# Optimization experiments

Hardware: AMD Instinct MI355X
Metric: run time of the kernel (lower is better)

## Reference

```python
import jax, jax.numpy as jnp
import numpy as np

B, T, D = 256, 300, 512


def setup_inputs() -> dict:
    key = jax.random.key(0)
    k1, k2, k3, k4 = jax.random.split(key, 4)
    x = jax.random.normal(k1, (B, T, D), dtype=jnp.float32)
    weights = jax.random.uniform(k2, (B, T, 1), dtype=jnp.float32)
    # learned params: D (log-variance vector, init zero-ish) and chol (upper-triangular, init ~identity)
    D_w = 0.01 * jax.random.normal(k3, (D,), dtype=jnp.float32)
    chol_w = jnp.eye(D, dtype=jnp.float32) + 0.01 * jnp.triu(
        jax.random.normal(k4, (D, D), dtype=jnp.float32), k=1)
    return {"x": x, "weights": weights, "D_w": D_w, "chol_w": chol_w}


def reference(x, weights, D_w, chol_w):
    # weighted first-order stats
    gamma = jnp.sum(x * weights, axis=1)                     # [B, D]
    N = jnp.sum(weights, axis=1, keepdims=True)              # [B, 1, 1]

    var_i = jnp.exp(D_w)                                     # [D]
    cov_i = (chol_w.T * var_i) @ chol_w                      # chol^T diag(var) chol, SPD [D, D]
    prec_i = jnp.linalg.inv(cov_i)[None]                     # [1, D, D]

    eye = jnp.eye(D, dtype=x.dtype)[None]                    # [1, D, D]
    prec = eye + N * prec_i                                  # [B, D, D]

    cov = jnp.linalg.inv(prec)                               # batched inverse [B, D, D]
    cov = 0.5 * (cov + jnp.transpose(cov, (0, 2, 1)))        # symmetrize

    # K.batch_dot(gamma, cov) with default axes contracts gamma dim1 with cov dim2
    mu = jnp.einsum('bd,bed->be', gamma, cov)                # [B, D]

    # upper Cholesky factor: cov = U^T U with U = L^T
    L = jnp.linalg.cholesky(cov)                             # lower [B, D, D]
    chol = jnp.transpose(L, (0, 2, 1))                       # upper [B, D, D]
    sigma = jnp.diagonal(chol, axis1=1, axis2=2)             # [B, D]
    chol = chol / sigma[:, :, None]                          # unit-diagonal rows
    logvar = 2.0 * jnp.log(sigma)                            # [B, D]
    return mu, logvar, chol
```

## Files before the change

### kernel.cpp

```cpp
#include <hip/hip_runtime.h>
#include <math.h>

#define Bn 256
#define Tn 300
#define Nn 512
#define NB 64
#define LDV 68
#define LDA 65

#define TOFF(i,j) ((size_t)((i)*NB)*Nn + (size_t)(j)*NB)

__device__ __forceinline__ void load_tile_f4(const float* __restrict__ g, int tid, float4 r[2]) {
#pragma unroll
  for (int t = 0; t < 2; t++) {
    int q = tid + 512 * t;
    int row = q >> 4, c4 = q & 15;
    r[t] = ((const float4*)(g + (size_t)row * Nn))[c4];
  }
}
__device__ __forceinline__ void store_stage(float* __restrict__ s, int tid, const float4 r[2]) {
#pragma unroll
  for (int t = 0; t < 2; t++) {
    int q = tid + 512 * t;
    int row = q >> 4, c4 = q & 15;
    *((float4*)(s + row * LDV + c4 * 4)) = r[t];
  }
}
__device__ __forceinline__ void mm_nt_sub(const float* __restrict__ sa, const float* __restrict__ sb,
                                          int tr, int tc, float acc[2][4]) {
#pragma unroll 2
  for (int k = 0; k < NB; k += 4) {
    float4 av[2], bv[4];
#pragma unroll
    for (int i = 0; i < 2; i++) av[i] = *(const float4*)(sa + (tr * 2 + i) * LDV + k);
#pragma unroll
    for (int j = 0; j < 4; j++) bv[j] = *(const float4*)(sb + (tc + 16 * j) * LDV + k);
#pragma unroll
    for (int i = 0; i < 2; i++)
#pragma unroll
      for (int j = 0; j < 4; j++)
        acc[i][j] -= av[i].x * bv[j].x + av[i].y * bv[j].y + av[i].z * bv[j].z + av[i].w * bv[j].w;
  }
}

__global__ __launch_bounds__(256) void k_gamma(const float* __restrict__ x,
                                               const float* __restrict__ w,
                                               float* __restrict__ gamma,
                                               float* __restrict__ Nsum) {
  int b = blockIdx.x, tid = threadIdx.x;
  const float2* xb = (const float2*)(x + (size_t)b * Tn * Nn);
  const float* wb = w + b * Tn;
  float gx = 0.f, gy = 0.f, ns = 0.f;
#pragma unroll 4
  for (int t = 0; t < Tn; t++) {
    float wt = wb[t];
    ns += wt;
    float2 v = xb[(size_t)t * 256 + tid];
    gx += v.x * wt;
    gy += v.y * wt;
  }
  float2 g2; g2.x = gx; g2.y = gy;
  ((float2*)(gamma + b * Nn))[tid] = g2;
  if (tid == 0) Nsum[b] = ns;
}

__global__ __launch_bounds__(256) void k_prepC(const float* __restrict__ Dw,
                                               const float* __restrict__ cholw,
                                               float* __restrict__ C) {
  int r = blockIdx.x, tid = threadIdx.x;
  float s = expf(0.5f * Dw[r]);
  for (int c = tid; c < Nn; c += 256)
    C[r * Nn + c] = (c >= r) ? s * cholw[r * Nn + c] : 0.f;
}

__global__ __launch_bounds__(256) void k_cct(const float* __restrict__ C,
                                             float* __restrict__ CCT) {
  __shared__ float Ci[32][33];
  __shared__ float Cj[32][33];
  int tid = threadIdx.x;
  int idx = blockIdx.x, ti = 0, tj;
  if (idx < 136) {
    while (idx >= 16 - ti) { idx -= 16 - ti; ti++; }
    tj = ti + idx;
  } else {
    ti = 2 * (idx - 136) + 1;
    tj = ti - 1;
  }
  int i0 = ti * 32, j0 = tj * 32;
  int m0 = (i0 > j0) ? i0 : j0;
  float acc[4] = {0.f, 0.f, 0.f, 0.f};
  int r = tid >> 3, c0 = tid & 7;
  for (int kt = m0; kt < Nn; kt += 32) {
    __syncthreads();
    for (int q = tid; q < 1024; q += 256) {
      int rr = q >> 5, cc = q & 31;
      Ci[rr][cc] = C[(size_t)(i0 + rr) * Nn + kt + cc];
      Cj[rr][cc] = C[(size_t)(j0 + rr) * Nn + kt + cc];
    }
    __syncthreads();
    for (int k = 0; k < 32; k++) {
      float a = Ci[r][k];
#pragma unroll
      for (int j = 0; j < 4; j++) acc[j] += a * Cj[c0 + 8 * j][k];
    }
  }
#pragma unroll
  for (int j = 0; j < 4; j++)
    CCT[(size_t)(i0 + r) * Nn + j0 + c0 + 8 * j] = acc[j];
}

__global__ __attribute__((amdgpu_waves_per_eu(2)))
__launch_bounds__(512) void k_factor(const float* __restrict__ CCT,
                                     const float* __restrict__ Nsum,
                                     float* __restrict__ AG) {
  const int b = blockIdx.x, tid = threadIdx.x;
  float* A = AG + (size_t)b * Nn * Nn;
  const float Nb = Nsum[b];
  __shared__ __align__(16) float sA[2][NB * LDV];
  __shared__ __align__(16) float sB[2][NB * LDV];
  __shared__ __align__(16) float sVd[NB * LDV];
  __shared__ float sAd[NB * LDA];
  __shared__ float sdg[NB];
  const int tr = tid >> 4, tc = tid & 15;
  float4 ra[2], rb[2];

  for (int j = 7; j >= 0; j--) {
    const int nst = 7 - j;
    float acc[2][4];
    {
      const float* T = CCT + TOFF(j, j);
#pragma unroll
      for (int i = 0; i < 2; i++) {
        const int r = tr * 2 + i;
#pragma unroll
        for (int jj = 0; jj < 4; jj++) {
          const int c = tc + 16 * jj;
          float v = T[(size_t)r * Nn + c];
          if (r == c) v += Nb;
          acc[i][jj] = v;
        }
      }
    }
    if (nst) {
      load_tile_f4(A + TOFF(j, j + 1), tid, ra);
      store_stage(sA[0], tid, ra);
    }
    __syncthreads();
    for (int kk = 0; kk < nst; kk++) {
      const int s = kk & 1;
      if (kk + 1 < nst) load_tile_f4(A + TOFF(j, j + 2 + kk), tid, ra);
      mm_nt_sub(sA[s], sA[s], tr, tc, acc);
      if (kk + 1 < nst) store_stage(sA[s ^ 1], tid, ra);
      __syncthreads();
    }
#pragma unroll
    for (int i = 0; i < 2; i++)
#pragma unroll
      for (int jj = 0; jj < 4; jj++)
        sAd[(tr * 2 + i) * LDA + tc + 16 * jj] = acc[i][jj];
    __syncthreads();
    {
      const int jj = tid & 63, i0 = tid >> 6;
      for (int c = NB - 1; c > 0; --c) {
        float invd = 1.0f / sAd[c * LDA + c];
        if (jj < c) {
          float t = sAd[jj * LDA + c] * invd;
          for (int i = i0; i <= jj; i += 8)
            sAd[i * LDA + jj] -= sAd[i * LDA + c] * t;
        }
        __syncthreads();
      }
      if (tid < NB) sdg[tid] = rsqrtf(sAd[tid * LDA + tid]);
      __syncthreads();
      for (int q = tid; q < NB * NB; q += 512) {
        int r = q >> 6, cc = q & 63;
        if (r <= cc) sAd[r * LDA + cc] *= sdg[cc];
      }
      __syncthreads();
    }
    for (int q = tid; q < NB * LDV; q += 512) sVd[q] = 0.f;
    __syncthreads();
    if (tid < NB) {
      const int c = tid;
      for (int r = c; r >= 0; r--) {
        float s2 = (r == c) ? 1.f : 0.f;
        for (int k = r + 1; k <= c; k++) s2 -= sAd[r * LDA + k] * sVd[k * LDV + c];
        sVd[r * LDV + c] = s2 / sAd[r * LDA + r];
      }
    }
    __syncthreads();
    {
      const int vr = (j < 7) ? 7 : 6, vc = (j < 7) ? j : 0;
      float* Vt = A + TOFF(vr, vc);
      for (int q = tid; q < NB * NB; q += 512) {
        int r = q >> 6, c = q & 63;
        Vt[(size_t)r * Nn + c] = sVd[r * LDV + c];
      }
    }
    for (int i = j - 1; i >= 0; i--) {
      float acc2[2][4];
      {
        const float* T = CCT + TOFF(i, j);
#pragma unroll
        for (int ii = 0; ii < 2; ii++)
#pragma unroll
          for (int jj = 0; jj < 4; jj++)
            acc2[ii][jj] = T[(size_t)(tr * 2 + ii) * Nn + tc + 16 * jj];
      }
      if (nst) {
        load_tile_f4(A + TOFF(i, j + 1), tid, ra);
        load_tile_f4(A + TOFF(j, j + 1), tid, rb);
        store_stage(sA[0], tid, ra);
        store_stage(sB[0], tid, rb);
      }
      __syncthreads();
      for (int kk = 0; kk < nst; kk++) {
        const int s = kk & 1;
        if (kk + 1 < nst) {
          load_tile_f4(A + TOFF(i, j + 2 + kk), tid, ra);
          load_tile_f4(A + TOFF(j, j + 2 + kk), tid, rb);
        }
        mm_nt_sub(sA[s], sB[s], tr, tc, acc2);
        if (kk + 1 < nst) { store_stage(sA[s ^ 1], tid, ra); store_stage(sB[s ^ 1], tid, rb); }
        __syncthreads();
      }
#pragma unroll
      for (int ii = 0; ii < 2; ii++)
#pragma unroll
        for (int jj = 0; jj < 4; jj++)
          sA[0][(tr * 2 + ii) * LDV + tc + 16 * jj] = acc2[ii][jj];
      __syncthreads();
      {
        float out[2][4] = {};
#pragma unroll 2
        for (int k = 0; k < NB; k += 4) {
          float4 av[2], bv[4];
#pragma unroll
          for (int ii = 0; ii < 2; ii++) av[ii] = *(const float4*)(sA[0] + (tr * 2 + ii) * LDV + k);
#pragma unroll
          for (int jj = 0; jj < 4; jj++) bv[jj] = *(const float4*)(sVd + (tc + 16 * jj) * LDV + k);
#pragma unroll
          for (int ii = 0; ii < 2; ii++)
#pragma unroll
            for (int jj = 0; jj < 4; jj++)
              out[ii][jj] += av[ii].x * bv[jj].x + av[ii].y * bv[jj].y +
                             av[ii].z * bv[jj].z + av[ii].w * bv[jj].w;
        }
        float* X = A + TOFF(i, j);
#pragma unroll
        for (int ii = 0; ii < 2; ii++)
#pragma unroll
          for (int jj = 0; jj < 4; jj++)
            X[(size_t)(tr * 2 + ii) * Nn + tc + 16 * jj] = out[ii][jj];
      }
      __syncthreads();
    }
  }
}

__global__ __attribute__((amdgpu_waves_per_eu(2)))
__launch_bounds__(512) void k_solve(const float* __restrict__ C,
                                    float* __restrict__ AG) {
  const int b = blockIdx.x, tid = threadIdx.x;
  float* A = AG + (size_t)b * Nn * Nn;
  __shared__ __align__(16) float sA[2][NB * LDV];
  __shared__ __align__(16) float sB[2][NB * LDV];
  __shared__ __align__(16) float sVd[NB * LDV];
  const int tr = tid >> 4, tc = tid & 15;
  float4 ra[2], rb[2];
  for (int R = 7; R >= 0; R--) {
    {
      const int vr = (R < 7) ? 7 : 6, vc = (R < 7) ? R : 0;
      const float* Vt = A + TOFF(vr, vc);
      __syncthreads();
      for (int q = tid; q < NB * NB; q += 512) {
        int r = q >> 6, c = q & 63;
        sVd[r * LDV + c] = Vt[(size_t)r * Nn + c];
      }
      __syncthreads();
    }
    for (int J = 7; J >= R; J--) {
      const int nst = J - R;
      float acc[2][4];
      {
        const float* T = C + TOFF(R, J);
#pragma unroll
        for (int ii = 0; ii < 2; ii++)
#pragma unroll
          for (int jj = 0; jj < 4; jj++)
            acc[ii][jj] = T[(size_t)(tr * 2 + ii) * Nn + tc + 16 * jj];
      }
      if (nst) {
        load_tile_f4(A + TOFF(R, R + 1), tid, ra);
        load_tile_f4(A + TOFF(R + 1, J), tid, rb);
      }
      __syncthreads();
      if (nst) { store_stage(sA[0], tid, ra); store_stage(sB[0], tid, rb); }
      __syncthreads();
      for (int kk = 0; kk < nst; kk++) {
        const int s = kk & 1;
        if (kk + 1 < nst) {
          load_tile_f4(A + TOFF(R, R + 2 + kk), tid, ra);
          load_tile_f4(A + TOFF(R + 2 + kk, J), tid, rb);
        }
#pragma unroll 2
        for (int k = 0; k < NB; k += 4) {
          float a4[2][4];
#pragma unroll
          for (int ii = 0; ii < 2; ii++) {
            float4 t = *(const float4*)(sA[s] + (tr * 2 + ii) * LDV + k);
            a4[ii][0] = t.x; a4[ii][1] = t.y; a4[ii][2] = t.z; a4[ii][3] = t.w;
          }
#pragma unroll
          for (int k2 = 0; k2 < 4; k2++) {
            float bb[4];
#pragma unroll
            for (int jj = 0; jj < 4; jj++) bb[jj] = sB[s][(k + k2) * LDV + tc + 16 * jj];
#pragma unroll
            for (int ii = 0; ii < 2; ii++)
#pragma unroll
              for (int jj = 0; jj < 4; jj++) acc[ii][jj] -= a4[ii][k2] * bb[jj];
          }
        }
        if (kk + 1 < nst) { store_stage(sA[s ^ 1], tid, ra); store_stage(sB[s ^ 1], tid, rb); }
        __syncthreads();
      }
#pragma unroll
      for (int ii = 0; ii < 2; ii++)
#pragma unroll
        for (int jj = 0; jj < 4; jj++)
          sA[0][(tr * 2 + ii) * LDV + tc + 16 * jj] = acc[ii][jj];
      __syncthreads();
      {
        float out[2][4] = {};
#pragma unroll 2
        for (int k = 0; k < NB; k += 4) {
          float v4[2][4];
#pragma unroll
          for (int ii = 0; ii < 2; ii++) {
            float4 t = *(const float4*)(sVd + (tr * 2 + ii) * LDV + k);
            v4[ii][0] = t.x; v4[ii][1] = t.y; v4[ii][2] = t.z; v4[ii][3] = t.w;
          }
#pragma unroll
          for (int k2 = 0; k2 < 4; k2++) {
            float bb[4];
#pragma unroll
            for (int jj = 0; jj < 4; jj++) bb[jj] = sA[0][(k + k2) * LDV + tc + 16 * jj];
#pragma unroll
            for (int ii = 0; ii < 2; ii++)
#pragma unroll
              for (int jj = 0; jj < 4; jj++) out[ii][jj] += v4[ii][k2] * bb[jj];
          }
        }
        float* G = A + TOFF(R, J);
#pragma unroll
        for (int ii = 0; ii < 2; ii++)
#pragma unroll
          for (int jj = 0; jj < 4; jj++)
            G[(size_t)(tr * 2 + ii) * Nn + tc + 16 * jj] = out[ii][jj];
      }
      __syncthreads();
    }
  }
}

__global__ __launch_bounds__(512) void k_finish(const float* __restrict__ gam,
                                                float* __restrict__ mu,
                                                float* __restrict__ logvar,
                                                float* __restrict__ cholG) {
  int b = blockIdx.x, tid = threadIdx.x;
  float* A = cholG + (size_t)b * Nn * Nn;
  __shared__ float gsh[Nn];
  __shared__ float mup[8][Nn];
  for (int c = tid; c < Nn; c += 512) gsh[c] = gam[b * Nn + c];
  __syncthreads();
  int w = tid >> 6, l = tid & 63;
  float mua[8] = {0.f, 0.f, 0.f, 0.f, 0.f, 0.f, 0.f, 0.f};
  for (int i = w; i < Nn; i += 8) {
    const size_t rowo = (size_t)i * Nn;
    float v[8];
    float s = 0.f;
#pragma unroll
    for (int j = 0; j < 8; j++) {
      int c = (j << 6) + l;
      v[j] = A[rowo + c];
      if (c >= i) s += v[j] * gsh[c];
    }
#pragma unroll
    for (int off = 32; off > 0; off >>= 1) s += __shfl_xor(s, off, 64);
    float d = A[rowo + i];
    float rinv = 1.f / d;
    if (l == 0) logvar[b * Nn + i] = 2.f * logf(d);
#pragma unroll
    for (int j = 0; j < 8; j++) {
      int c = (j << 6) + l;
      if (c >= i) mua[j] += v[j] * s;
      float o = (c > i) ? v[j] * rinv : (c == i ? 1.f : 0.f);
      A[rowo + c] = o;
    }
  }
#pragma unroll
  for (int j = 0; j < 8; j++) mup[w][(j << 6) + l] = mua[j];
  __syncthreads();
  for (int c = tid; c < Nn; c += 512)
    mu[b * Nn + c] = mup[0][c] + mup[1][c] + mup[2][c] + mup[3][c] +
                     mup[4][c] + mup[5][c] + mup[6][c] + mup[7][c];
}

extern "C" void kernel_launch(void* const* d_in, const int* in_sizes, int n_in,
                              void* d_out, int out_size, void* d_ws, size_t ws_size,
                              hipStream_t stream) {
  const float* x = (const float*)d_in[0];
  const float* w = (const float*)d_in[1];
  const float* Dw = (const float*)d_in[2];
  const float* cholw = (const float*)d_in[3];
  float* out = (float*)d_out;
  float* mu = out;
  float* logvar = out + Bn * Nn;
  float* chol = out + 2 * Bn * Nn;
  float* gamma = mu;
  float* Nsum = logvar;
  float* Cm = (float*)d_ws;
  float* CCT = Cm + Nn * Nn;
  (void)in_sizes; (void)n_in; (void)out_size; (void)ws_size;

  k_gamma<<<Bn, 256, 0, stream>>>(x, w, gamma, Nsum);
  k_prepC<<<Nn, 256, 0, stream>>>(Dw, cholw, Cm);
  k_cct<<<144, 256, 0, stream>>>(Cm, CCT);
  k_factor<<<Bn, 512, 0, stream>>>(CCT, Nsum, chol);
  k_solve<<<Bn, 512, 0, stream>>>(Cm, chol);
  k_finish<<<Bn, 512, 0, stream>>>(gamma, mu, logvar, chol);
}
```

Before: 2.255 ms.

## Process two off-diagonal tiles per pass in blocked factor and solve kernels

The blocked inverse-factor and triangular-solve kernels now handle two 64x64 output tiles per loop iteration. Each shared staged tile (the diagonal-row panel in k_factor, the A panel in k_solve) is reused across both accumulations, which cuts barrier count and shared loads per tile. The cost is higher register pressure from double accumulators and more shared memory, since a third staging double-buffer is added and sAd is aliased onto sA1. The trailing __syncthreads after each output write was removed, which relies on the next iteration's barriers to order shared-memory reuse.

```diff
diff --git a/kernel.cpp b/kernel.cpp
--- a/kernel.cpp
+++ b/kernel.cpp
@@ -40,6 +40,115 @@
 #pragma unroll
       for (int j = 0; j < 4; j++)
         acc[i][j] -= av[i].x * bv[j].x + av[i].y * bv[j].y + av[i].z * bv[j].z + av[i].w * bv[j].w;
+  }
+}
+__device__ __forceinline__ void mm_nt_sub2(const float* __restrict__ sa1, const float* __restrict__ sa2,
+                                           const float* __restrict__ sb,
+                                           int tr, int tc, float accA[2][4], float accB[2][4]) {
+#pragma unroll 2
+  for (int k = 0; k < NB; k += 4) {
+    float4 a1[2], a2[2], bv[4];
+#pragma unroll
+    for (int i = 0; i < 2; i++) {
+      a1[i] = *(const float4*)(sa1 + (tr * 2 + i) * LDV + k);
+      a2[i] = *(const float4*)(sa2 + (tr * 2 + i) * LDV + k);
+    }
+#pragma unroll
+    for (int j = 0; j < 4; j++) bv[j] = *(const float4*)(sb + (tc + 16 * j) * LDV + k);
+#pragma unroll
+    for (int i = 0; i < 2; i++)
+#pragma unroll
+      for (int j = 0; j < 4; j++) {
+        accA[i][j] -= a1[i].x * bv[j].x + a1[i].y * bv[j].y + a1[i].z * bv[j].z + a1[i].w * bv[j].w;
+        accB[i][j] -= a2[i].x * bv[j].x + a2[i].y * bv[j].y + a2[i].z * bv[j].z + a2[i].w * bv[j].w;
+      }
+  }
+}
+__device__ __forceinline__ void mm_nt_pos2(const float* __restrict__ t1, const float* __restrict__ t2,
+                                           const float* __restrict__ vd, bool u2,
+                                           int tr, int tc, float o1[2][4], float o2[2][4]) {
+#pragma unroll 2
+  for (int k = 0; k < NB; k += 4) {
+    float4 a1[2], a2[2], bv[4];
+#pragma unroll
+    for (int i = 0; i < 2; i++) {
+      a1[i] = *(const float4*)(t1 + (tr * 2 + i) * LDV + k);
+      if (u2) a2[i] = *(const float4*)(t2 + (tr * 2 + i) * LDV + k);
+    }
+#pragma unroll
+    for (int j = 0; j < 4; j++) bv[j] = *(const float4*)(vd + (tc + 16 * j) * LDV + k);
+#pragma unroll
+    for (int i = 0; i < 2; i++)
+#pragma unroll
+      for (int j = 0; j < 4; j++) {
+        o1[i][j] += a1[i].x * bv[j].x + a1[i].y * bv[j].y + a1[i].z * bv[j].z + a1[i].w * bv[j].w;
+        if (u2)
+          o2[i][j] += a2[i].x * bv[j].x + a2[i].y * bv[j].y + a2[i].z * bv[j].z + a2[i].w * bv[j].w;
+      }
+  }
+}
+__device__ __forceinline__ void mm_ab_sub2(const float* __restrict__ sa, const float* __restrict__ b1,
+                                           const float* __restrict__ b2, bool u2,
+                                           int tr, int tc, float acc1[2][4], float acc2[2][4]) {
+#pragma unroll 2
+  for (int k = 0; k < NB; k += 4) {
+    float a4[2][4];
+#pragma unroll
+    for (int ii = 0; ii < 2; ii++) {
+      float4 t = *(const float4*)(sa + (tr * 2 + ii) * LDV + k);
+      a4[ii][0] = t.x; a4[ii][1] = t.y; a4[ii][2] = t.z; a4[ii][3] = t.w;
+    }
+#pragma unroll
+    for (int k2 = 0; k2 < 4; k2++) {
+      float bb1[4];
+#pragma unroll
+      for (int jj = 0; jj < 4; jj++) bb1[jj] = b1[(k + k2) * LDV + tc + 16 * jj];
+#pragma unroll
+      for (int ii = 0; ii < 2; ii++)
+#pragma unroll
+        for (int jj = 0; jj < 4; jj++) acc1[ii][jj] -= a4[ii][k2] * bb1[jj];
+      if (u2) {
+        float bb2[4];
+#pragma unroll
+        for (int jj = 0; jj < 4; jj++) bb2[jj] = b2[(k + k2) * LDV + tc + 16 * jj];
+#pragma unroll
+        for (int ii = 0; ii < 2; ii++)
+#pragma unroll
+          for (int jj = 0; jj < 4; jj++) acc2[ii][jj] -= a4[ii][k2] * bb2[jj];
+      }
+    }
+  }
+}
+__device__ __forceinline__ void mm_vd2(const float* __restrict__ vd, const float* __restrict__ t1,
+                                       const float* __restrict__ t2, bool u2,
+                                       int tr, int tc, float o1[2][4], float o2[2][4]) {
+#pragma unroll 2
+  for (int k = 0; k < NB; k += 4) {
+    float v4[2][4];
+#pragma unroll
+    for (int ii = 0; ii < 2; ii++) {
+      float4 t = *(const float4*)(vd + (tr * 2 + ii) * LDV + k);
+      v4[ii][0] = t.x; v4[ii][1] = t.y; v4[ii][2] = t.z; v4[ii][3] = t.w;
+    }
+#pragma unroll
+    for (int k2 = 0; k2 < 4; k2++) {
+      float bb1[4];
+#pragma unroll
+      for (int jj = 0; jj < 4; jj++) bb1[jj] = t1[(k + k2) * LDV + tc + 16 * jj];
+#pragma unroll
+      for (int ii = 0; ii < 2; ii++)
+#pragma unroll
+        for (int jj = 0; jj < 4; jj++) o1[ii][jj] += v4[ii][k2] * bb1[jj];
+      if (u2) {
+        float bb2[4];
+#pragma unroll
+        for (int jj = 0; jj < 4; jj++) bb2[jj] = t2[(k + k2) * LDV + tc + 16 * jj];
+#pragma unroll
+        for (int ii = 0; ii < 2; ii++)
+#pragma unroll
+          for (int jj = 0; jj < 4; jj++) o2[ii][jj] += v4[ii][k2] * bb2[jj];
+      }
+    }
   }
 }
 
@@ -116,13 +225,14 @@
   const int b = blockIdx.x, tid = threadIdx.x;
   float* A = AG + (size_t)b * Nn * Nn;
   const float Nb = Nsum[b];
-  __shared__ __align__(16) float sA[2][NB * LDV];
+  __shared__ __align__(16) float sA1[2][NB * LDV];
+  __shared__ __align__(16) float sA2[2][NB * LDV];
   __shared__ __align__(16) float sB[2][NB * LDV];
   __shared__ __align__(16) float sVd[NB * LDV];
-  __shared__ float sAd[NB * LDA];
   __shared__ float sdg[NB];
+  float* sAd = &sA1[0][0];
   const int tr = tid >> 4, tc = tid & 15;
-  float4 ra[2], rb[2];
+  float4 ra1[2], ra2[2], rb[2];
 
   for (int j = 7; j >= 0; j--) {
     const int nst = 7 - j;
@@ -141,16 +251,15 @@
         }
       }
     }
-    if (nst) {
-      load_tile_f4(A + TOFF(j, j + 1), tid, ra);
-      store_stage(sA[0], tid, ra);
-    }
+    if (nst) load_tile_f4(A + TOFF(j, j + 1), tid, ra1);
+    __syncthreads();
+    if (nst) store_stage(sB[0], tid, ra1);
     __syncthreads();
     for (int kk = 0; kk < nst; kk++) {
       const int s = kk & 1;
-      if (kk + 1 < nst) load_tile_f4(A + TOFF(j, j + 2 + kk), tid, ra);
-      mm_nt_sub(sA[s], sA[s], tr, tc, acc);
-      if (kk + 1 < nst) store_stage(sA[s ^ 1], tid, ra);
+      if (kk + 1 < nst) load_tile_f4(A + TOFF(j, j + 2 + kk), tid, ra1);
+      mm_nt_sub(sB[s], sB[s], tr, tc, acc);
+      if (kk + 1 < nst) store_stage(sB[s ^ 1], tid, ra1);
       __syncthreads();
     }
 #pragma unroll
@@ -197,63 +306,76 @@
         Vt[(size_t)r * Nn + c] = sVd[r * LDV + c];
       }
     }
-    for (int i = j - 1; i >= 0; i--) {
-      float acc2[2][4];
+    int i = j - 1;
+    while (i >= 0) {
+      const bool two = (i >= 1);
+      float accA[2][4], accB[2][4];
       {
-        const float* T = CCT + TOFF(i, j);
+        const float* Ta = CCT + TOFF(i, j);
+        const float* Tb = two ? (CCT + TOFF(i - 1, j)) : Ta;
 #pragma unroll
         for (int ii = 0; ii < 2; ii++)
 #pragma unroll
-          for (int jj = 0; jj < 4; jj++)
-            acc2[ii][jj] = T[(size_t)(tr * 2 + ii) * Nn + tc + 16 * jj];
+          for (int jj = 0; jj < 4; jj++) {
+            accA[ii][jj] = Ta[(size_t)(tr * 2 + ii) * Nn + tc + 16 * jj];
+            accB[ii][jj] = two ? Tb[(size_t)(tr * 2 + ii) * Nn + tc + 16 * jj] : 0.f;
+          }
       }
       if (nst) {
-        load_tile_f4(A + TOFF(i, j + 1), tid, ra);
+        load_tile_f4(A + TOFF(i, j + 1), tid, ra1);
+        if (two) load_tile_f4(A + TOFF(i - 1, j + 1), tid, ra2);
         load_tile_f4(A + TOFF(j, j + 1), tid, rb);
-        store_stage(sA[0], tid, ra);
+      }
+      __syncthreads();
+      if (nst) {
+        store_stage(sA1[0], tid, ra1);
+        if (two) store_stage(sA2[0], tid, ra2);
         store_stage(sB[0], tid, rb);
       }
       __syncthreads();
       for (int kk = 0; kk < nst; kk++) {
         const int s = kk & 1;
         if (kk + 1 < nst) {
-          load_tile_f4(A + TOFF(i, j + 2 + kk), tid, ra);
+          load_tile_f4(A + TOFF(i, j + 2 + kk), tid, ra1);
+          if (two) load_tile_f4(A + TOFF(i - 1, j + 2 + kk), tid, ra2);
           load_tile_f4(A + TOFF(j, j + 2 + kk), tid, rb);
         }
-        mm_nt_sub(sA[s], sB[s], tr, tc, acc2);
-        if (kk + 1 < nst) { store_stage(sA[s ^ 1], tid, ra); store_stage(sB[s ^ 1], tid, rb); }
+        if (two) mm_nt_sub2(sA1[s], sA2[s], sB[s], tr, tc, accA, accB);
+        else     mm_nt_sub(sA1[s], sB[s], tr, tc, accA);
+        if (kk + 1 < nst) {
+          store_stage(sA1[s ^ 1], tid, ra1);
+          if (two) store_stage(sA2[s ^ 1], tid, ra2);
+          store_stage(sB[s ^ 1], tid, rb);
+        }
         __syncthreads();
       }
 #pragma unroll
       for (int ii = 0; ii < 2; ii++)
 #pragma unroll
-        for (int jj = 0; jj < 4; jj++)
-          sA[0][(tr * 2 + ii) * LDV + tc + 16 * jj] = acc2[ii][jj];
+        for (int jj = 0; jj < 4; jj++) {
+          sA1[0][(tr * 2 + ii) * LDV + tc + 16 * jj] = accA[ii][jj];
+          if (two) sA2[0][(tr * 2 + ii) * LDV + tc + 16 * jj] = accB[ii][jj];
+        }
       __syncthreads();
       {
-        float out[2][4] = {};
-#pragma unroll 2
-        for (int k = 0; k < NB; k += 4) {
-          float4 av[2], bv[4];
-#pragma unroll
-          for (int ii = 0; ii < 2; ii++) av[ii] = *(const float4*)(sA[0] + (tr * 2 + ii) * LDV + k);
-#pragma unroll
-          for (int jj = 0; jj < 4; jj++) bv[jj] = *(const float4*)(sVd + (tc + 16 * jj) * LDV + k);
+        float oA[2][4] = {}, oB[2][4] = {};
+        mm_nt_pos2(sA1[0], sA2[0], sVd, two, tr, tc, oA, oB);
+        float* Xa = A + TOFF(i, j);
+#pragma unroll
+        for (int ii = 0; ii < 2; ii++)
+#pragma unroll
+          for (int jj = 0; jj < 4; jj++)
+            Xa[(size_t)(tr * 2 + ii) * Nn + tc + 16 * jj] = oA[ii][jj];
+        if (two) {
+          float* Xb = A + TOFF(i - 1, j);
 #pragma unroll
           for (int ii = 0; ii < 2; ii++)
 #pragma unroll
             for (int jj = 0; jj < 4; jj++)
-              out[ii][jj] += av[ii].x * bv[jj].x + av[ii].y * bv[jj].y +
-                             av[ii].z * bv[jj].z + av[ii].w * bv[jj].w;
-        }
-        float* X = A + TOFF(i, j);
-#pragma unroll
-        for (int ii = 0; ii < 2; ii++)
-#pragma unroll
-          for (int jj = 0; jj < 4; jj++)
-            X[(size_t)(tr * 2 + ii) * Nn + tc + 16 * jj] = out[ii][jj];
-      }
-      __syncthreads();
+              Xb[(size_t)(tr * 2 + ii) * Nn + tc + 16 * jj] = oB[ii][jj];
+        }
+      }
+      i -= 2;
     }
   }
 }
@@ -264,10 +386,11 @@
   const int b = blockIdx.x, tid = threadIdx.x;
   float* A = AG + (size_t)b * Nn * Nn;
   __shared__ __align__(16) float sA[2][NB * LDV];
-  __shared__ __align__(16) float sB[2][NB * LDV];
+  __shared__ __align__(16) float sB1[2][NB * LDV];
+  __shared__ __align__(16) float sB2[2][NB * LDV];
   __shared__ __align__(16) float sVd[NB * LDV];
   const int tr = tid >> 4, tc = tid & 15;
-  float4 ra[2], rb[2];
+  float4 ra[2], rb1[2], rb2[2];
   for (int R = 7; R >= 0; R--) {
     {
       const int vr = (R < 7) ? 7 : 6, vc = (R < 7) ? R : 0;
@@ -279,87 +402,77 @@
       }
       __syncthreads();
     }
-    for (int J = 7; J >= R; J--) {
-      const int nst = J - R;
-      float acc[2][4];
+    int J = 7;
+    while (J >= R) {
+      const bool two = (J - 1 >= R);
+      const int nst1 = J - R;
+      const int nst2 = J - 1 - R;
+      float acc1[2][4], acc2[2][4];
       {
-        const float* T = C + TOFF(R, J);
+        const float* T1 = C + TOFF(R, J);
+        const float* T2 = two ? (C + TOFF(R, J - 1)) : T1;
 #pragma unroll
         for (int ii = 0; ii < 2; ii++)
 #pragma unroll
+          for (int jj = 0; jj < 4; jj++) {
+            acc1[ii][jj] = T1[(size_t)(tr * 2 + ii) * Nn + tc + 16 * jj];
+            acc2[ii][jj] = two ? T2[(size_t)(tr * 2 + ii) * Nn + tc + 16 * jj] : 0.f;
+          }
+      }
+      if (nst1) {
+        load_tile_f4(A + TOFF(R, R + 1), tid, ra);
+        load_tile_f4(A + TOFF(R + 1, J), tid, rb1);
+        if (two && nst2 > 0) load_tile_f4(A + TOFF(R + 1, J - 1), tid, rb2);
+      }
+      __syncthreads();
+      if (nst1) {
+        store_stage(sA[0], tid, ra);
+        store_stage(sB1[0], tid, rb1);
+        if (two && nst2 > 0) store_stage(sB2[0], tid, rb2);
+      }
+      __syncthreads();
+      for (int kk = 0; kk < nst1; kk++) {
+        const int s = kk & 1;
+        if (kk + 1 < nst1) {
+          load_tile_f4(A + TOFF(R, R + 2 + kk), tid, ra);
+          load_tile_f4(A + TOFF(R + 2 + kk, J), tid, rb1);
+          if (two && kk + 1 < nst2) load_tile_f4(A + TOFF(R + 2 + kk, J - 1), tid, rb2);
+        }
+        mm_ab_sub2(sA[s], sB1[s], sB2[s], two && (kk < nst2), tr, tc, acc1, acc2);
+        if (kk + 1 < nst1) {
+          store_stage(sA[s ^ 1], tid, ra);
+          store_stage(sB1[s ^ 1], tid, rb1);
+          if (two && kk + 1 < nst2) store_stage(sB2[s ^ 1], tid, rb2);
+        }
+        __syncthreads();
+      }
+#pragma unroll
+      for (int ii = 0; ii < 2; ii++)
+#pragma unroll
+        for (int jj = 0; jj < 4; jj++) {
+          sB1[0][(tr * 2 + ii) * LDV + tc + 16 * jj] = acc1[ii][jj];
+          if (two) sB2[0][(tr * 2 + ii) * LDV + tc + 16 * jj] = acc2[ii][jj];
+        }
+      __syncthreads();
+      {
+        float o1[2][4] = {}, o2[2][4] = {};
+        mm_vd2(sVd, sB1[0], sB2[0], two, tr, tc, o1, o2);
+        float* G1 = A + TOFF(R, J);
+#pragma unroll
+        for (int ii = 0; ii < 2; ii++)
+#pragma unroll
           for (int jj = 0; jj < 4; jj++)
-            acc[ii][jj] = T[(size_t)(tr * 2 + ii) * Nn + tc + 16 * jj];
-      }
-      if (nst) {
-        load_tile_f4(A + TOFF(R, R + 1), tid, ra);
-        load_tile_f4(A + TOFF(R + 1, J), tid, rb);
-      }
-      __syncthreads();
-      if (nst) { store_stage(sA[0], tid, ra); store_stage(sB[0], tid, rb); }
-      __syncthreads();
-      for (int kk = 0; kk < nst; kk++) {
-        const int s = kk & 1;
-        if (kk + 1 < nst) {
-          load_tile_f4(A + TOFF(R, R + 2 + kk), tid, ra);
-          load_tile_f4(A + TOFF(R + 2 + kk, J), tid, rb);
-        }
-#pragma unroll 2
-        for (int k = 0; k < NB; k += 4) {
-          float a4[2][4];
-#pragma unroll
-          for (int ii = 0; ii < 2; ii++) {
-            float4 t = *(const float4*)(sA[s] + (tr * 2 + ii) * LDV + k);
-            a4[ii][0] = t.x; a4[ii][1] = t.y; a4[ii][2] = t.z; a4[ii][3] = t.w;
-          }
-#pragma unroll
-          for (int k2 = 0; k2 < 4; k2++) {
-            float bb[4];
-#pragma unroll
-            for (int jj = 0; jj < 4; jj++) bb[jj] = sB[s][(k + k2) * LDV + tc + 16 * jj];
-#pragma unroll
-            for (int ii = 0; ii < 2; ii++)
-#pragma unroll
-              for (int jj = 0; jj < 4; jj++) acc[ii][jj] -= a4[ii][k2] * bb[jj];
-          }
-        }
-        if (kk + 1 < nst) { store_stage(sA[s ^ 1], tid, ra); store_stage(sB[s ^ 1], tid, rb); }
-        __syncthreads();
-      }
-#pragma unroll
-      for (int ii = 0; ii < 2; ii++)
-#pragma unroll
-        for (int jj = 0; jj < 4; jj++)
-          sA[0][(tr * 2 + ii) * LDV + tc + 16 * jj] = acc[ii][jj];
-      __syncthreads();
-      {
-        float out[2][4] = {};
-#pragma unroll 2
-        for (int k = 0; k < NB; k += 4) {
-          float v4[2][4];
-#pragma unroll
-          for (int ii = 0; ii < 2; ii++) {
-            float4 t = *(const float4*)(sVd + (tr * 2 + ii) * LDV + k);
-            v4[ii][0] = t.x; v4[ii][1] = t.y; v4[ii][2] = t.z; v4[ii][3] = t.w;
-          }
-#pragma unroll
-          for (int k2 = 0; k2 < 4; k2++) {
-            float bb[4];
-#pragma unroll
-            for (int jj = 0; jj < 4; jj++) bb[jj] = sA[0][(k + k2) * LDV + tc + 16 * jj];
-#pragma unroll
-            for (int ii = 0; ii < 2; ii++)
-#pragma unroll
-              for (int jj = 0; jj < 4; jj++) out[ii][jj] += v4[ii][k2] * bb[jj];
-          }
-        }
-        float* G = A + TOFF(R, J);
-#pragma unroll
-        for (int ii = 0; ii < 2; ii++)
-#pragma unroll
-          for (int jj = 0; jj < 4; jj++)
-            G[(size_t)(tr * 2 + ii) * Nn + tc + 16 * jj] = out[ii][jj];
-      }
-      __syncthreads();
+            G1[(size_t)(tr * 2 + ii) * Nn + tc + 16 * jj] = o1[ii][jj];
+        if (two) {
+          float* G2 = A + TOFF(R, J - 1);
+#pragma unroll
+          for (int ii = 0; ii < 2; ii++)
+#pragma unroll
+            for (int jj = 0; jj < 4; jj++)
+              G2[(size_t)(tr * 2 + ii) * Nn + tc + 16 * jj] = o2[ii][jj];
+        }
+      }
+      J -= 2;
     }
   }
 }
```

Measured after the change: 2.374 ms. 5.3% more time.
